# Kernel optimization log

Hardware: AMD Instinct MI355X
Metric: run time of the kernel (lower is better)

Reference implementation:

```python
import jax, jax.numpy as jnp
import numpy as np

B, D_IN, D_H = 16384, 512, 1024


def _glorot(key, out_d, in_d):
    lim = 1.0 / np.sqrt(in_d)
    return jax.random.uniform(key, (out_d, in_d), minval=-lim, maxval=lim, dtype=jnp.float32)


def setup_inputs() -> dict:
    key = jax.random.key(0)
    ks = jax.random.split(key, 16)
    inp = {
        "x_t": jax.random.normal(ks[0], (B, D_IN), dtype=jnp.float32),
        "delta_t": jax.random.uniform(ks[1], (B, 1), dtype=jnp.float32),
        "h_prev": jax.random.normal(ks[2], (B, D_H), dtype=jnp.float32),
        # torch nn.Linear weights are [out, in]; y = x @ W.T
        "W_sh": _glorot(ks[3], D_H, D_H),
        "W_sx": _glorot(ks[4], D_H, D_IN),
        "W_st": _glorot(ks[5], D_H, 1),
        "b_s": jnp.zeros((D_H,), jnp.float32),
        "WTh": _glorot(ks[6], D_H, D_H),
        "WTx": _glorot(ks[7], D_H, D_IN),
        "WTs": _glorot(ks[8], D_H, D_H),
        "b_T": jnp.zeros((D_H,), jnp.float32),
        "W_rh": _glorot(ks[9], D_H, D_H),
        "W_rx": _glorot(ks[10], D_H, D_IN),
        "b_r": jnp.zeros((D_H,), jnp.float32),
        "W_zh": _glorot(ks[11], D_H, D_H),
        "W_zx": _glorot(ks[12], D_H, D_IN),
        "b_z": jnp.zeros((D_H,), jnp.float32),
        "W_h": _glorot(ks[13], D_H, D_H),
        "W_x": _glorot(ks[14], D_H, D_IN),
        "b": jnp.zeros((D_H,), jnp.float32),
    }
    return inp


def reference(x_t, delta_t, h_prev,
              W_sh, W_sx, W_st, b_s,
              WTh, WTx, WTs, b_T,
              W_rh, W_rx, b_r,
              W_zh, W_zx, b_z,
              W_h, W_x, b):
    lin = lambda x, W: x @ W.T  # nn.Linear(bias=False)
    s_t = jnp.tanh(lin(h_prev, W_sh) + lin(x_t, W_sx) + lin(delta_t, W_st) + b_s)
    T_t = jax.nn.sigmoid(lin(h_prev, WTh) + lin(x_t, WTx) + lin(s_t, WTs) + b_T)
    r_t = jax.nn.sigmoid(lin(h_prev, W_rh) + lin(x_t, W_rx) + b_r)
    z_t = jax.nn.sigmoid(lin(h_prev, W_zh) + lin(x_t, W_zx) + b_z)
    h_tilde = jnp.tanh(lin(r_t * h_prev, W_h) + lin(x_t, W_x) + b)
    h_t = (1.0 - z_t) * (T_t * h_prev) + z_t * h_tilde
    return h_t
```

## Files before the change

### kernel.cpp

```cpp
#include <hip/hip_runtime.h>
#include <stdint.h>

#define AS1 __attribute__((address_space(1)))
#define AS3 __attribute__((address_space(3)))

typedef unsigned short US;
typedef __bf16 bf16x8 __attribute__((ext_vector_type(8)));
typedef float f32x4 __attribute__((ext_vector_type(4)));
typedef int intx4 __attribute__((ext_vector_type(4)));

static constexpr int Bsz = 16384;
static constexpr int DIN = 512;
static constexpr int DH  = 1024;
static constexpr int LDA = 2560;
static constexpr int LDR = 1536;

__device__ __forceinline__ US f2bf(float f) {
  unsigned u = __float_as_uint(f);
  u += 0x7fffu + ((u >> 16) & 1u);
  return (US)(u >> 16);
}
__device__ __forceinline__ float bf2f(US u) { return __uint_as_float(((unsigned)u) << 16); }
__device__ __forceinline__ float sigm(float x) { return 1.f / (1.f + __expf(-x)); }
__device__ __forceinline__ float tanh_f(float x) { return 1.f - 2.f / (1.f + __expf(2.f * x)); }

__device__ __forceinline__ intx4 dsr128(unsigned addr) {
  intx4 r;
  asm volatile("ds_read_b128 %0, %1" : "=v"(r) : "v"(addr));
  return r;
}

#define BARR  __builtin_amdgcn_s_barrier()
#define SB0   __builtin_amdgcn_sched_barrier(0)
#define LGKM0 { asm volatile("s_waitcnt lgkmcnt(0)"); __builtin_amdgcn_sched_barrier(0); }
#define VMC6  { asm volatile("s_waitcnt vmcnt(6)"); __builtin_amdgcn_sched_barrier(0); }
#define VMC0  { asm volatile("s_waitcnt vmcnt(0)"); __builtin_amdgcn_sched_barrier(0); }

__global__ void pack_A(const float* __restrict__ h, const float* __restrict__ x,
                       US* __restrict__ Ab, US* __restrict__ RHx) {
  const int total = Bsz * 384;
  for (int idx = blockIdx.x * blockDim.x + threadIdx.x; idx < total;
       idx += gridDim.x * blockDim.x) {
    int row = idx / 384;
    int c = (idx - row * 384) * 4;
    const float* src = (c < DH) ? (h + (size_t)row * DH + c)
                                : (x + (size_t)row * DIN + (c - DH));
    float4 v = *(const float4*)src;
    ushort4 o;
    o.x = f2bf(v.x); o.y = f2bf(v.y); o.z = f2bf(v.z); o.w = f2bf(v.w);
    *(ushort4*)(Ab + (size_t)row * LDA + c) = o;
    if (c >= DH) *(ushort4*)(RHx + (size_t)row * LDR + c) = o;
  }
}

struct WSlot { const float* src; US* dst; int n4; int ksh; int ld; int co; };
struct WBatch { WSlot s[11]; };
__global__ void conv_w(WBatch b) {
  WSlot sl = b.s[blockIdx.y];
  const int mask = (1 << sl.ksh) - 1;
  for (int i = blockIdx.x * blockDim.x + threadIdx.x; i < sl.n4;
       i += gridDim.x * blockDim.x) {
    float4 v = *(const float4*)(sl.src + (size_t)i * 4);
    ushort4 o;
    o.x = f2bf(v.x); o.y = f2bf(v.y); o.z = f2bf(v.z); o.w = f2bf(v.w);
    int r = i >> sl.ksh;
    int cc = (i & mask) * 4;
    *(ushort4*)(sl.dst + (size_t)r * sl.ld + sl.co + cc) = o;
  }
}

template <int EPI, int NBLK>
__global__ __launch_bounds__(512, 2) void gemm8(
    const US* __restrict__ A, int lda,
    const US* __restrict__ W, int ldw, int nt,
    const float* __restrict__ bias0, const float* __restrict__ bias1,
    const float* __restrict__ bias2,
    const void* aux0, const void* aux1, const void* aux2,
    void* out0, int ldo0, void* out1, void* out2) {
  __shared__ __align__(16) US As[2][256 * 64];
  __shared__ __align__(16) US Bs[2][256 * 64];

  const int tid  = threadIdx.x;
  const int lane = tid & 63;
  const int w    = tid >> 6;
  const int wr   = w >> 2;
  const int wc   = w & 3;
  const int quad = lane >> 4, l15 = lane & 15;
  const int sw8  = l15 & 7;
  const int lrow = lane >> 3;
  const int scc  = (lane & 7) ^ (lrow & 7);

  const int p = blockIdx.x;
  const int c = p & 7, q = p >> 3;
  const int nIdx = q % NBLK, mIdx = c * 8 + q / NBLK;
  const int mBase = mIdx * 256, nBase = nIdx * 256;

  f32x4 acc[8][4];
#pragma unroll
  for (int i = 0; i < 8; i++)
#pragma unroll
    for (int j = 0; j < 4; j++) acc[i][j] = f32x4{0.f, 0.f, 0.f, 0.f};

  const unsigned aBase = (unsigned)(uintptr_t)&As[0][0];
  const unsigned bBase = (unsigned)(uintptr_t)&Bs[0][0];
  const unsigned arB = (unsigned)((wr * 128 + l15) * 128);
  const unsigned brB = (unsigned)((wc * 64 + l15) * 128);
  const unsigned kc0 = (unsigned)((quad ^ sw8) * 16);

  const size_t aRowS = (size_t)(mBase + w * 8 + lrow) * lda;
  const size_t wRowS = (size_t)(nBase + w * 8 + lrow) * ldw;
  const int sccOff = scc * 8;

#define STAGE_A(d, hh, co)                                                       \
  { const US* g = A + aRowS + (size_t)(hh) * 128 * lda + (co) + sccOff;          \
    __builtin_amdgcn_global_load_lds((AS1 const void*)g,                         \
        (AS3 void*)&As[d][((hh)*128 + w * 8) * 64], 16, 0, 0);                   \
    __builtin_amdgcn_global_load_lds((AS1 const void*)(g + (size_t)64 * lda),    \
        (AS3 void*)&As[d][((hh)*128 + 64 + w * 8) * 64], 16, 0, 0); }
#define STAGE_B(d, hh, co)                                                       \
  { const US* g = W + wRowS + (size_t)(hh) * 128 * ldw + (co) + sccOff;          \
    __builtin_amdgcn_global_load_lds((AS1 const void*)g,                         \
        (AS3 void*)&Bs[d][((hh)*128 + w * 8) * 64], 16, 0, 0);                   \
    __builtin_amdgcn_global_load_lds((AS1 const void*)(g + (size_t)64 * ldw),    \
        (AS3 void*)&Bs[d][((hh)*128 + 64 + w * 8) * 64], 16, 0, 0); }

#define READ_A(AF, mh)                                                           \
  _Pragma("unroll")                                                              \
  for (int i = 0; i < 4; ++i)                                                    \
    _Pragma("unroll")                                                            \
    for (int ks = 0; ks < 2; ++ks)                                               \
      AF[i][ks] = dsr128(aC + arB + (mh)*8192u + (unsigned)i * 2048u +           \
                         (kc0 ^ (unsigned)(ks << 6)));
#define READ_B(BSET, nh)                                                         \
  _Pragma("unroll")                                                              \
  for (int j = 0; j < 2; ++j)                                                    \
    _Pragma("unroll")                                                            \
    for (int ks = 0; ks < 2; ++ks)                                               \
      BSET[j][ks] = dsr128(bC + brB + (nh)*4096u + (unsigned)j * 2048u +         \
                           (kc0 ^ (unsigned)(ks << 6)));
#define MFMA_Q(AF, mh, BSET, nh)                                                 \
  _Pragma("unroll")                                                              \
  for (int ks = 0; ks < 2; ++ks)                                                 \
    _Pragma("unroll")                                                            \
    for (int i = 0; i < 4; ++i)                                                  \
      _Pragma("unroll")                                                          \
      for (int j = 0; j < 2; ++j)                                                \
        acc[(mh)*4 + i][(nh)*2 + j] = __builtin_amdgcn_mfma_f32_16x16x32_bf16(   \
            __builtin_bit_cast(bf16x8, AF[i][ks]),                               \
            __builtin_bit_cast(bf16x8, BSET[j][ks]),                             \
            acc[(mh)*4 + i][(nh)*2 + j], 0, 0, 0);

  STAGE_A(0, 0, 0); STAGE_A(0, 1, 0); STAGE_B(0, 0, 0); STAGE_B(0, 1, 0);
  STAGE_B(1, 0, 64); STAGE_B(1, 1, 64); STAGE_A(1, 0, 64);
  VMC6;
  BARR;

  intx4 af0[4][2], af1[4][2], b0[2][2], b1[2][2];
  int cur = 0;

  for (int t = 0; t < nt; ++t, cur ^= 1) {
    const unsigned aC = aBase + (unsigned)cur * 32768u;
    const unsigned bC = bBase + (unsigned)cur * 32768u;
    const int nxt = cur ^ 1;
    const bool s1 = (t + 1 < nt), s2 = (t + 2 < nt);
    const int co1 = (t + 1) * 64, co2 = (t + 2) * 64;
    READ_A(af0, 0);
    READ_B(b0, 0);
    if (s1) STAGE_A(nxt, 1, co1);
    BARR;
    LGKM0;
    __builtin_amdgcn_s_setprio(1);
    MFMA_Q(af0, 0, b0, 0);
    __builtin_amdgcn_s_setprio(0);
    BARR;
    READ_B(b1, 1);
    BARR;
    LGKM0;
    __builtin_amdgcn_s_setprio(1);
    MFMA_Q(af0, 0, b1, 1);
    __builtin_amdgcn_s_setprio(0);
    BARR;
    READ_A(af1, 1);
    if (s2) STAGE_B(cur, 0, co2);
    BARR;
    LGKM0;
    __builtin_amdgcn_s_setprio(1);
    MFMA_Q(af1, 1, b0, 0);
    __builtin_amdgcn_s_setprio(0);
    BARR;
    if (s2) { STAGE_B(cur, 1, co2); STAGE_A(cur, 0, co2); }
    BARR;
    __builtin_amdgcn_s_setprio(1);
    MFMA_Q(af1, 1, b1, 1);
    __builtin_amdgcn_s_setprio(0);
    if (s1) {
      if (s2) { VMC6; } else { VMC0; }
      BARR;
    }
  }
#undef STAGE_A
#undef STAGE_B
#undef READ_A
#undef READ_B
#undef MFMA_Q

#pragma unroll
  for (int im = 0; im < 8; ++im) {
#pragma unroll
    for (int jn = 0; jn < 4; ++jn) {
      const int col = nBase + wc * 64 + jn * 16 + l15;
      if constexpr (EPI == 0) {
        const int g = nIdx >> 2;
        const int colg = col & 1023;
        const float* bp = (g == 0) ? bias0 : (g == 1) ? bias1 : bias2;
        const float bv = bp[colg];
        const float* delta = (const float*)aux0;
        const float* wst   = (const float*)aux1;
        const float* hp    = (const float*)aux2;
#pragma unroll
        for (int r = 0; r < 4; ++r) {
          const int row = mBase + wr * 128 + im * 16 + quad * 4 + r;
          float v = acc[im][jn][r] + bv;
          if (g == 0) {
            v += delta[row] * wst[colg];
            ((US*)out0)[(size_t)row * ldo0 + colg] = f2bf(tanh_f(v));
          } else if (g == 1) {
            float rr = sigm(v);
            ((US*)out1)[(size_t)row * LDR + colg] =
                f2bf(rr * hp[(size_t)row * DH + colg]);
          } else {
            ((US*)out2)[(size_t)row * DH + colg] = f2bf(sigm(v));
          }
        }
      } else if constexpr (EPI == 3) {
        const float bv = bias0[col];
#pragma unroll
        for (int r = 0; r < 4; ++r) {
          const int row = mBase + wr * 128 + im * 16 + quad * 4 + r;
          float v = acc[im][jn][r] + bv;
          ((US*)out0)[(size_t)row * ldo0 + col] = f2bf(tanh_f(v));
        }
      } else {
        const float bv = bias0[col];
        const float* hp = (const float*)aux0;
        const US* Zp = (const US*)aux1;
        const US* Hp = (const US*)aux2;
#pragma unroll
        for (int r = 0; r < 4; ++r) {
          const int row = mBase + wr * 128 + im * 16 + quad * 4 + r;
          float v = acc[im][jn][r] + bv;
          float T = sigm(v);
          size_t o = (size_t)row * DH + col;
          float z = bf2f(Zp[o]), ht = bf2f(Hp[o]);
          float h = hp[o];
          ((float*)out0)[(size_t)row * ldo0 + col] = (1.f - z) * (T * h) + z * ht;
        }
      }
    }
  }
}

extern "C" void kernel_launch(void* const* d_in, const int* in_sizes, int n_in,
                              void* d_out, int out_size, void* d_ws, size_t ws_size,
                              hipStream_t stream) {
  const float* x_t   = (const float*)d_in[0];
  const float* delta = (const float*)d_in[1];
  const float* h_prev= (const float*)d_in[2];
  const float* W_sh  = (const float*)d_in[3];
  const float* W_sx  = (const float*)d_in[4];
  const float* W_st  = (const float*)d_in[5];
  const float* b_s   = (const float*)d_in[6];
  const float* WTh   = (const float*)d_in[7];
  const float* WTx   = (const float*)d_in[8];
  const float* WTs   = (const float*)d_in[9];
  const float* b_T   = (const float*)d_in[10];
  const float* W_rh  = (const float*)d_in[11];
  const float* W_rx  = (const float*)d_in[12];
  const float* b_r   = (const float*)d_in[13];
  const float* W_zh  = (const float*)d_in[14];
  const float* W_zx  = (const float*)d_in[15];
  const float* b_z   = (const float*)d_in[16];
  const float* W_h   = (const float*)d_in[17];
  const float* W_x   = (const float*)d_in[18];
  const float* b_    = (const float*)d_in[19];
  float* out = (float*)d_out;

  char* ws = (char*)d_ws;
  US* Ab  = (US*)ws;              size_t off = (size_t)Bsz * LDA * 2;
  US* RH  = (US*)(ws + off);      off += (size_t)Bsz * LDR * 2;
  US* Zb  = (US*)(ws + off);      off += (size_t)Bsz * DH * 2;
  US* HTb = (US*)(ws + off);      off += (size_t)Bsz * DH * 2;
  US* bWsrz = (US*)(ws + off);    off += (size_t)3072 * 1536 * 2;
  US* bWT   = (US*)(ws + off);    off += (size_t)DH * 2560 * 2;
  US* bWh   = (US*)(ws + off);    off += (size_t)DH * 1536 * 2;

  pack_A<<<dim3(8192), 256, 0, stream>>>(h_prev, x_t, Ab, RH);
  WBatch wb;
  const int n4h = DH * DH / 4, n4x = DH * DIN / 4;
  US* bWr = bWsrz + (size_t)1024 * 1536;
  US* bWz = bWsrz + (size_t)2048 * 1536;
  wb.s[0]  = {W_sh, bWsrz, n4h, 8, 1536, 0};
  wb.s[1]  = {W_sx, bWsrz, n4x, 7, 1536, 1024};
  wb.s[2]  = {W_rh, bWr,   n4h, 8, 1536, 0};
  wb.s[3]  = {W_rx, bWr,   n4x, 7, 1536, 1024};
  wb.s[4]  = {W_zh, bWz,   n4h, 8, 1536, 0};
  wb.s[5]  = {W_zx, bWz,   n4x, 7, 1536, 1024};
  wb.s[6]  = {WTh,  bWT,   n4h, 8, 2560, 0};
  wb.s[7]  = {WTx,  bWT,   n4x, 7, 2560, 1024};
  wb.s[8]  = {WTs,  bWT,   n4h, 8, 2560, 1536};
  wb.s[9]  = {W_h,  bWh,   n4h, 8, 1536, 0};
  wb.s[10] = {W_x,  bWh,   n4x, 7, 1536, 1024};
  conv_w<<<dim3(512, 11), 256, 0, stream>>>(wb);

  gemm8<0, 12><<<dim3(768), 512, 0, stream>>>(
      Ab, LDA, bWsrz, 1536, 24, b_s, b_r, b_z,
      delta, W_st, h_prev, (void*)(Ab + 1536), LDA, (void*)RH, (void*)Zb);
  gemm8<3, 4><<<dim3(256), 512, 0, stream>>>(
      RH, LDR, bWh, 1536, 24, b_, nullptr, nullptr,
      nullptr, nullptr, nullptr, (void*)HTb, DH, nullptr, nullptr);
  gemm8<4, 4><<<dim3(256), 512, 0, stream>>>(
      Ab, LDA, bWT, 2560, 40, b_T, nullptr, nullptr,
      h_prev, Zb, HTb, (void*)out, DH, nullptr, nullptr);
}
```

Before: 678.9 us.

## Rework GEMM LDS pipeline with compiler-scheduled reads and single A fragment set

Replaces the inline-asm ds_read_b128 LDS reads and the manual lgkmcnt(0) waits with plain C++ vector loads, so the compiler inserts the waits itself. The two A-fragment register sets are merged into one to cut VGPR pressure. The global-to-LDS staging schedule also changes: both A halves of the next tile are now staged within the current iteration instead of one half running two tiles ahead, with the vmcnt thresholds adjusted to match. This shortens A prefetch depth and gives up explicit control over wait placement in exchange for fewer registers and less forced stalling.

```diff
diff --git a/kernel.cpp b/kernel.cpp
--- a/kernel.cpp
+++ b/kernel.cpp
@@ -7,7 +7,6 @@
 typedef unsigned short US;
 typedef __bf16 bf16x8 __attribute__((ext_vector_type(8)));
 typedef float f32x4 __attribute__((ext_vector_type(4)));
-typedef int intx4 __attribute__((ext_vector_type(4)));
 
 static constexpr int Bsz = 16384;
 static constexpr int DIN = 512;
@@ -24,17 +23,8 @@
 __device__ __forceinline__ float sigm(float x) { return 1.f / (1.f + __expf(-x)); }
 __device__ __forceinline__ float tanh_f(float x) { return 1.f - 2.f / (1.f + __expf(2.f * x)); }
 
-__device__ __forceinline__ intx4 dsr128(unsigned addr) {
-  intx4 r;
-  asm volatile("ds_read_b128 %0, %1" : "=v"(r) : "v"(addr));
-  return r;
-}
-
 #define BARR  __builtin_amdgcn_s_barrier()
 #define SB0   __builtin_amdgcn_sched_barrier(0)
-#define LGKM0 { asm volatile("s_waitcnt lgkmcnt(0)"); __builtin_amdgcn_sched_barrier(0); }
-#define VMC6  { asm volatile("s_waitcnt vmcnt(6)"); __builtin_amdgcn_sched_barrier(0); }
-#define VMC0  { asm volatile("s_waitcnt vmcnt(0)"); __builtin_amdgcn_sched_barrier(0); }
 
 __global__ void pack_A(const float* __restrict__ h, const float* __restrict__ x,
                        US* __restrict__ Ab, US* __restrict__ RHx) {
@@ -101,12 +91,6 @@
 #pragma unroll
     for (int j = 0; j < 4; j++) acc[i][j] = f32x4{0.f, 0.f, 0.f, 0.f};
 
-  const unsigned aBase = (unsigned)(uintptr_t)&As[0][0];
-  const unsigned bBase = (unsigned)(uintptr_t)&Bs[0][0];
-  const unsigned arB = (unsigned)((wr * 128 + l15) * 128);
-  const unsigned brB = (unsigned)((wc * 64 + l15) * 128);
-  const unsigned kc0 = (unsigned)((quad ^ sw8) * 16);
-
   const size_t aRowS = (size_t)(mBase + w * 8 + lrow) * lda;
   const size_t wRowS = (size_t)(nBase + w * 8 + lrow) * ldw;
   const int sccOff = scc * 8;
@@ -124,21 +108,21 @@
     __builtin_amdgcn_global_load_lds((AS1 const void*)(g + (size_t)64 * ldw),    \
         (AS3 void*)&Bs[d][((hh)*128 + 64 + w * 8) * 64], 16, 0, 0); }
 
-#define READ_A(AF, mh)                                                           \
+#define READ_A(mh)                                                               \
   _Pragma("unroll")                                                              \
   for (int i = 0; i < 4; ++i)                                                    \
     _Pragma("unroll")                                                            \
     for (int ks = 0; ks < 2; ++ks)                                               \
-      AF[i][ks] = dsr128(aC + arB + (mh)*8192u + (unsigned)i * 2048u +           \
-                         (kc0 ^ (unsigned)(ks << 6)));
+      af[i][ks] = *(const bf16x8*)&As[cur][(wr * 128 + (mh)*64 + i * 16 + l15)   \
+                                          * 64 + (((ks * 4 + quad) ^ sw8) * 8)];
 #define READ_B(BSET, nh)                                                         \
   _Pragma("unroll")                                                              \
   for (int j = 0; j < 2; ++j)                                                    \
     _Pragma("unroll")                                                            \
     for (int ks = 0; ks < 2; ++ks)                                               \
-      BSET[j][ks] = dsr128(bC + brB + (nh)*4096u + (unsigned)j * 2048u +         \
-                           (kc0 ^ (unsigned)(ks << 6)));
-#define MFMA_Q(AF, mh, BSET, nh)                                                 \
+      BSET[j][ks] = *(const bf16x8*)&Bs[cur][(wc * 64 + (nh)*32 + j * 16 + l15)  \
+                                            * 64 + (((ks * 4 + quad) ^ sw8) * 8)];
+#define MFMA_Q(mh, BSET, nh)                                                     \
   _Pragma("unroll")                                                              \
   for (int ks = 0; ks < 2; ++ks)                                                 \
     _Pragma("unroll")                                                            \
@@ -146,56 +130,53 @@
       _Pragma("unroll")                                                          \
       for (int j = 0; j < 2; ++j)                                                \
         acc[(mh)*4 + i][(nh)*2 + j] = __builtin_amdgcn_mfma_f32_16x16x32_bf16(   \
-            __builtin_bit_cast(bf16x8, AF[i][ks]),                               \
-            __builtin_bit_cast(bf16x8, BSET[j][ks]),                             \
-            acc[(mh)*4 + i][(nh)*2 + j], 0, 0, 0);
+            af[i][ks], BSET[j][ks], acc[(mh)*4 + i][(nh)*2 + j], 0, 0, 0);
 
   STAGE_A(0, 0, 0); STAGE_A(0, 1, 0); STAGE_B(0, 0, 0); STAGE_B(0, 1, 0);
-  STAGE_B(1, 0, 64); STAGE_B(1, 1, 64); STAGE_A(1, 0, 64);
-  VMC6;
+  if (nt > 1) { STAGE_B(1, 0, 64); STAGE_B(1, 1, 64); }
+  if (nt > 1) __builtin_amdgcn_s_waitcnt(0x0f74);
+  else        __builtin_amdgcn_s_waitcnt(0x0f70);
   BARR;
-
-  intx4 af0[4][2], af1[4][2], b0[2][2], b1[2][2];
+  SB0;
+
+  bf16x8 af[4][2], b0[2][2], b1[2][2];
   int cur = 0;
 
   for (int t = 0; t < nt; ++t, cur ^= 1) {
-    const unsigned aC = aBase + (unsigned)cur * 32768u;
-    const unsigned bC = bBase + (unsigned)cur * 32768u;
     const int nxt = cur ^ 1;
-    const bool s1 = (t + 1 < nt), s2 = (t + 2 < nt);
     const int co1 = (t + 1) * 64, co2 = (t + 2) * 64;
-    READ_A(af0, 0);
+    READ_A(0);
     READ_B(b0, 0);
-    if (s1) STAGE_A(nxt, 1, co1);
-    BARR;
-    LGKM0;
+    if (t + 1 < nt) STAGE_A(nxt, 0, co1);
+    BARR;
     __builtin_amdgcn_s_setprio(1);
-    MFMA_Q(af0, 0, b0, 0);
+    MFMA_Q(0, b0, 0);
     __builtin_amdgcn_s_setprio(0);
     BARR;
     READ_B(b1, 1);
-    BARR;
-    LGKM0;
+    if (t + 1 < nt) STAGE_A(nxt, 1, co1);
+    BARR;
     __builtin_amdgcn_s_setprio(1);
-    MFMA_Q(af0, 0, b1, 1);
+    MFMA_Q(0, b1, 1);
     __builtin_amdgcn_s_setprio(0);
     BARR;
-    READ_A(af1, 1);
-    if (s2) STAGE_B(cur, 0, co2);
-    BARR;
-    LGKM0;
+    READ_A(1);
+    if (t + 2 < nt) STAGE_B(cur, 0, co2);
+    BARR;
     __builtin_amdgcn_s_setprio(1);
-    MFMA_Q(af1, 1, b0, 0);
+    MFMA_Q(1, b0, 0);
     __builtin_amdgcn_s_setprio(0);
     BARR;
-    if (s2) { STAGE_B(cur, 1, co2); STAGE_A(cur, 0, co2); }
+    if (t + 2 < nt) STAGE_B(cur, 1, co2);
     BARR;
     __builtin_amdgcn_s_setprio(1);
-    MFMA_Q(af1, 1, b1, 1);
+    MFMA_Q(1, b1, 1);
     __builtin_amdgcn_s_setprio(0);
-    if (s1) {
-      if (s2) { VMC6; } else { VMC0; }
+    if (t + 1 < nt) {
+      if (t + 2 < nt) __builtin_amdgcn_s_waitcnt(0x0f74);
+      else            __builtin_amdgcn_s_waitcnt(0x0f70);
       BARR;
+      SB0;
     }
   }
 #undef STAGE_A
```

Result: slower. 769.1 us (+13.3%).
